# Performance work log

Hardware: AMD Instinct MI355X
Metric: run time of the kernel (lower is better)

Reference implementation:

```python
import jax, jax.numpy as jnp
import numpy as np

B, S, D, H, F, V = 64, 64, 512, 8, 2048, 8192
L = 6
ENC_C = 2048  # InceptionV3 feature channels
NEG_INF = jnp.float32(-jnp.inf)


def _layernorm(x, g, b, eps=1e-3):
    mu = jnp.mean(x, axis=-1, keepdims=True)
    var = jnp.var(x, axis=-1, keepdims=True)
    return (x - mu) * jax.lax.rsqrt(var + eps) * g + b


def _mha(q_in, kv_in, Wq, Wk, Wv, Wo, causal=False):
    Bq, Sq, Dm = q_in.shape
    Sk = kv_in.shape[1]
    dh = Dm // H
    q = (q_in @ Wq).reshape(Bq, Sq, H, dh)
    k = (kv_in @ Wk).reshape(Bq, Sk, H, dh)
    v = (kv_in @ Wv).reshape(Bq, Sk, H, dh)
    scores = jnp.einsum('bqhd,bkhd->bhqk', q, k) / jnp.sqrt(jnp.float32(dh))
    if causal:
        mask = jnp.tril(jnp.ones((Sq, Sk), dtype=bool))
        scores = jnp.where(mask, scores, jnp.float32(-1e9))
    a = jax.nn.softmax(scores, axis=-1)
    o = jnp.einsum('bhqk,bkhd->bqhd', a, v).reshape(Bq, Sq, Dm)
    return o @ Wo


def replacement_mask(targets):
    # out[b,i,v] = -inf iff some j<=i has targets[b,j]==v and v!=0
    valid = (targets != 0)[..., None].astype(jnp.float32)  # (B,S,1)
    oh = jax.nn.one_hot(targets, V, dtype=jnp.float32) * valid  # (B,S,V)
    seen = jnp.cumsum(oh, axis=1) > 0
    return jnp.where(seen, NEG_INF, jnp.float32(0.0))


def setup_inputs() -> dict:
    key = jax.random.key(0)
    ks = jax.random.split(key, 32)
    n = lambda i, shp, sc=0.02: jax.random.normal(ks[i], shp, jnp.float32) * sc
    inp = {
        'enc_feat': jax.random.normal(ks[0], (B, 8, 8, ENC_C), jnp.float32),
        'targets': jax.random.randint(ks[1], (B, S), 0, V, jnp.int32),
        'conv_w': n(2, (ENC_C, D)), 'conv_b': jnp.zeros((D,), jnp.float32),
        'tok_emb': n(3, (V, D)), 'pos_emb': n(4, (S, D)),
        'Wq_s': n(5, (L, D, D)), 'Wk_s': n(6, (L, D, D)),
        'Wv_s': n(7, (L, D, D)), 'Wo_s': n(8, (L, D, D)),
        'Wq_c': n(9, (L, D, D)), 'Wk_c': n(10, (L, D, D)),
        'Wv_c': n(11, (L, D, D)), 'Wo_c': n(12, (L, D, D)),
        'W1': n(13, (L, D, F)), 'fb1': jnp.zeros((L, F), jnp.float32),
        'W2': n(14, (L, F, D)), 'fb2': jnp.zeros((L, D), jnp.float32),
        'g1': jnp.ones((L, D), jnp.float32), 'be1': jnp.zeros((L, D), jnp.float32),
        'g2': jnp.ones((L, D), jnp.float32), 'be2': jnp.zeros((L, D), jnp.float32),
        'g3': jnp.ones((L, D), jnp.float32), 'be3': jnp.zeros((L, D), jnp.float32),
        'Wout': n(15, (D, V)), 'bout': jnp.zeros((V,), jnp.float32),
    }
    return inp


def reference(enc_feat, conv_w, conv_b, tok_emb, pos_emb,
              Wq_s, Wk_s, Wv_s, Wo_s, Wq_c, Wk_c, Wv_c, Wo_c,
              W1, fb1, W2, fb2, g1, be1, g2, be2, g3, be3,
              Wout, bout, targets):
    # 1x1 conv == per-pixel matmul, then flatten spatial -> (B, 64, D)
    enc = enc_feat.reshape(B, -1, ENC_C) @ conv_w + conv_b
    # decoder: token + positional embedding
    x = tok_emb[targets] + pos_emb[None, :, :]
    for l in range(L):
        a1 = _mha(x, x, Wq_s[l], Wk_s[l], Wv_s[l], Wo_s[l], causal=True)
        x = _layernorm(x + a1, g1[l], be1[l])
        a2 = _mha(x, enc, Wq_c[l], Wk_c[l], Wv_c[l], Wo_c[l])
        x = _layernorm(x + a2, g2[l], be2[l])
        ff = jax.nn.relu(x @ W1[l] + fb1[l]) @ W2[l] + fb2[l]
        x = _layernorm(x + ff, g3[l], be3[l])
    logits = x @ Wout + bout
    return logits + replacement_mask(targets)
```

## Files before the change

### kernel.cpp

```cpp
#include <hip/hip_runtime.h>
#include <cstdint>
#include <cstddef>

#define SS   64
#define BB   64
#define DM   512
#define NH   8
#define DH   64
#define FF   2048
#define VV   8192
#define LL   6
#define ENCC 2048
#define MR   4096

#define MASK_SENTINEL -3.0e38f

typedef unsigned short u16;
typedef __attribute__((ext_vector_type(8))) short bf16x8;
typedef __attribute__((ext_vector_type(4))) float f32x4;

__device__ __forceinline__ u16 f2b(float f) {
    union { float f; uint32_t u; } c; c.f = f;
    uint32_t u = c.u;
    return (u16)((u + 0x7fffu + ((u >> 16) & 1u)) >> 16);
}
__device__ __forceinline__ float blo(uint32_t p) {
    union { uint32_t u; float f; } c; c.u = p << 16; return c.f;
}
__device__ __forceinline__ float bhi(uint32_t p) {
    union { uint32_t u; float f; } c; c.u = p & 0xffff0000u; return c.f;
}

#define GLL(g, l) __builtin_amdgcn_global_load_lds( \
    (const __attribute__((address_space(1))) void*)(g), \
    (__attribute__((address_space(3))) void*)(l), 16, 0, 0)

#define WAITV2 asm volatile("s_waitcnt vmcnt(2)" ::: "memory")
#define WAITV3 asm volatile("s_waitcnt vmcnt(3)" ::: "memory")
#define WAITV4 asm volatile("s_waitcnt vmcnt(4)" ::: "memory")
#define WAITV0 asm volatile("s_waitcnt vmcnt(0)" ::: "memory")
#define WAITL0 asm volatile("s_waitcnt lgkmcnt(0)" ::: "memory")

template<int BMT, int BNT>
__global__ __launch_bounds__(256) void gemm_bf16(
    const u16* __restrict__ A, const u16* __restrict__ BT,
    const float* __restrict__ bias, u16* __restrict__ Cb,
    int K, int ldc, int relu)
{
    constexpr int WNW = (BNT == 128) ? 2 : 1;
    constexpr int WMW = 4 / WNW;
    constexpr int WM = BMT / WMW;
    constexpr int AI = WM / 16;
    constexpr int AG = BMT / 64;
    constexpr int BG = BNT / 64;
    constexpr int G  = AG + BG;
    constexpr int TILE = (BMT + BNT) * 32;
    __shared__ __align__(16) u16 smem[3 * TILE];
    const int tid = threadIdx.x;
    const int wave = tid >> 6, lane = tid & 63;

    const int m0 = blockIdx.y * BMT, n0 = blockIdx.x * BNT;
    const int srow = wave * 16 + (lane >> 2);
    const int scol = (lane & 3) * 8;
    const u16* Ap  = A  + (size_t)(m0 + srow) * K + scol;
    const u16* Bp  = BT + (size_t)(n0 + srow) * K + scol;
    const u16* Ap2 = Ap + (size_t)64 * K;
    const u16* Bp2 = Bp + (size_t)64 * K;
    const int aW = wave * 16 * 32;
    const int bW = BMT * 32 + wave * 16 * 32;

    const int wm = (BNT == 128) ? (wave >> 1) : wave;
    const int wn = (BNT == 128) ? (wave & 1) : 0;
    const int q = lane >> 4, mr = lane & 15;
    const int aRd = (wm * WM + mr) * 32 + q * 8;
    const int bRd = BMT * 32 + (wn * 64 + mr) * 32 + q * 8;

    f32x4 acc[AI][4];
    const f32x4 z = {0.f, 0.f, 0.f, 0.f};
#pragma unroll
    for (int i = 0; i < AI; i++)
#pragma unroll
        for (int j = 0; j < 4; j++) acc[i][j] = z;

#define STAGE(buf) do { \
        GLL(Ap, (buf) + aW); \
        if constexpr (AG == 2) GLL(Ap2, (buf) + aW + 64 * 32); \
        GLL(Bp, (buf) + bW); \
        if constexpr (BG == 2) GLL(Bp2, (buf) + bW + 64 * 32); \
        Ap += 32; Bp += 32; \
        if constexpr (AG == 2) Ap2 += 32; \
        if constexpr (BG == 2) Bp2 += 32; \
    } while (0)

    u16* rd = smem;
    u16* md = smem + TILE;
    u16* pf = smem + 2 * TILE;
    STAGE(rd);
    STAGE(md);
    const int NS = K >> 5;

    for (int k = 0; k < NS - 1; k++) {
        if constexpr (G == 2) WAITV2;
        else if constexpr (G == 3) WAITV3;
        else WAITV4;
        __builtin_amdgcn_s_barrier();
        bf16x8 af[AI], bfr[4];
#pragma unroll
        for (int i = 0; i < AI; i++) af[i]  = *(const bf16x8*)(rd + aRd + i * 16 * 32);
#pragma unroll
        for (int j = 0; j < 4; j++) bfr[j] = *(const bf16x8*)(rd + bRd + j * 16 * 32);
        WAITL0;
        __builtin_amdgcn_sched_barrier(0);
        if (k + 2 < NS) STAGE(pf);
#pragma unroll
        for (int i = 0; i < AI; i++)
#pragma unroll
            for (int j = 0; j < 4; j++)
                acc[i][j] = __builtin_amdgcn_mfma_f32_16x16x32_bf16(af[i], bfr[j], acc[i][j], 0, 0, 0);
        u16* t = rd; rd = md; md = pf; pf = t;
    }
    WAITV0;
    __builtin_amdgcn_s_barrier();
    {
        bf16x8 af[AI], bfr[4];
#pragma unroll
        for (int i = 0; i < AI; i++) af[i]  = *(const bf16x8*)(rd + aRd + i * 16 * 32);
#pragma unroll
        for (int j = 0; j < 4; j++) bfr[j] = *(const bf16x8*)(rd + bRd + j * 16 * 32);
#pragma unroll
        for (int i = 0; i < AI; i++)
#pragma unroll
            for (int j = 0; j < 4; j++)
                acc[i][j] = __builtin_amdgcn_mfma_f32_16x16x32_bf16(af[i], bfr[j], acc[i][j], 0, 0, 0);
    }
    __syncthreads();
#undef STAGE

    float* ep = (float*)smem + wave * 1024;
    const int lq = lane >> 4, lmr = lane & 15;
    const int colb = n0 + wn * 64 + lmr * 4;
    float4 b4 = make_float4(0.f, 0.f, 0.f, 0.f);
    if (bias) b4 = *(const float4*)(bias + colb);
#pragma unroll
    for (int i = 0; i < AI; i++) {
#pragma unroll
        for (int j = 0; j < 4; j++)
#pragma unroll
            for (int r = 0; r < 4; r++)
                ep[(q * 4 + r) * 64 + j * 16 + mr] = acc[i][j][r];
        __syncthreads();
#pragma unroll
        for (int p = 0; p < 4; p++) {
            const int lr = p * 4 + lq;
            float4 v = *(const float4*)(ep + lr * 64 + lmr * 4);
            v.x += b4.x; v.y += b4.y; v.z += b4.z; v.w += b4.w;
            if (relu) {
                v.x = fmaxf(v.x, 0.f); v.y = fmaxf(v.y, 0.f);
                v.z = fmaxf(v.z, 0.f); v.w = fmaxf(v.w, 0.f);
            }
            uint2 pk;
            pk.x = (uint32_t)f2b(v.x) | ((uint32_t)f2b(v.y) << 16);
            pk.y = (uint32_t)f2b(v.z) | ((uint32_t)f2b(v.w) << 16);
            const int row = m0 + wm * WM + i * 16 + lr;
            *(uint2*)(Cb + (size_t)row * ldc + colb) = pk;
        }
        __syncthreads();
    }
}

__global__ __launch_bounds__(256) void gemm_logits_mfma(
    const u16* __restrict__ A, const u16* __restrict__ BT,
    const float* __restrict__ bias, const int* __restrict__ fo,
    float* __restrict__ C, int K)
{
    constexpr int TILE = 256 * 32;
    __shared__ __align__(16) u16 smem[3 * TILE];
    const int tid = threadIdx.x;
    const int wave = tid >> 6, lane = tid & 63;
    const int m0 = blockIdx.y * 128, n0 = blockIdx.x * 128;

    const int srow = wave * 16 + (lane >> 2);
    const int scol = (lane & 3) * 8;
    const u16* Ap  = A  + (size_t)(m0 + srow) * K + scol;
    const u16* Bp  = BT + (size_t)(n0 + srow) * K + scol;
    const u16* Ap2 = Ap + (size_t)64 * K;
    const u16* Bp2 = Bp + (size_t)64 * K;
    const int aW = wave * 16 * 32;
    const int bW = 128 * 32 + wave * 16 * 32;

    const int wm = wave >> 1, wn = wave & 1;
    const int q = lane >> 4, mr = lane & 15;
    const int aRd = (wm * 64 + mr) * 32 + q * 8;
    const int bRd = 128 * 32 + (wn * 64 + mr) * 32 + q * 8;

    f32x4 acc[4][4];
    const f32x4 z = {0.f, 0.f, 0.f, 0.f};
#pragma unroll
    for (int i = 0; i < 4; i++)
#pragma unroll
        for (int j = 0; j < 4; j++) acc[i][j] = z;

#define STAGE4(buf) do { \
        GLL(Ap,  (buf) + aW); \
        GLL(Ap2, (buf) + aW + 64 * 32); \
        GLL(Bp,  (buf) + bW); \
        GLL(Bp2, (buf) + bW + 64 * 32); \
        Ap += 32; Ap2 += 32; Bp += 32; Bp2 += 32; \
    } while (0)

    u16* rd = smem;
    u16* md = smem + TILE;
    u16* pf = smem + 2 * TILE;
    STAGE4(rd);
    STAGE4(md);
    const int NS = K >> 5;

    for (int k = 0; k < NS - 1; k++) {
        WAITV4;
        __builtin_amdgcn_s_barrier();
        bf16x8 af[4], bfr[4];
#pragma unroll
        for (int i = 0; i < 4; i++) af[i]  = *(const bf16x8*)(rd + aRd + i * 16 * 32);
#pragma unroll
        for (int j = 0; j < 4; j++) bfr[j] = *(const bf16x8*)(rd + bRd + j * 16 * 32);
        WAITL0;
        __builtin_amdgcn_sched_barrier(0);
        if (k + 2 < NS) STAGE4(pf);
#pragma unroll
        for (int i = 0; i < 4; i++)
#pragma unroll
            for (int j = 0; j < 4; j++)
                acc[i][j] = __builtin_amdgcn_mfma_f32_16x16x32_bf16(af[i], bfr[j], acc[i][j], 0, 0, 0);
        u16* t = rd; rd = md; md = pf; pf = t;
    }
    WAITV0;
    __builtin_amdgcn_s_barrier();
    {
        bf16x8 af[4], bfr[4];
#pragma unroll
        for (int i = 0; i < 4; i++) af[i]  = *(const bf16x8*)(rd + aRd + i * 16 * 32);
#pragma unroll
        for (int j = 0; j < 4; j++) bfr[j] = *(const bf16x8*)(rd + bRd + j * 16 * 32);
#pragma unroll
        for (int i = 0; i < 4; i++)
#pragma unroll
            for (int j = 0; j < 4; j++)
                acc[i][j] = __builtin_amdgcn_mfma_f32_16x16x32_bf16(af[i], bfr[j], acc[i][j], 0, 0, 0);
    }
    __syncthreads();
#undef STAGE4

    float* ep = (float*)smem + wave * 1024;
    const int lq = lane >> 4, lmr = lane & 15;
    const int colb = n0 + wn * 64 + lmr * 4;
    const float4 b4 = *(const float4*)(bias + colb);
#pragma unroll
    for (int i = 0; i < 4; i++) {
#pragma unroll
        for (int j = 0; j < 4; j++)
#pragma unroll
            for (int r = 0; r < 4; r++)
                ep[(q * 4 + r) * 64 + j * 16 + mr] = acc[i][j][r];
        __syncthreads();
#pragma unroll
        for (int p = 0; p < 4; p++) {
            const int lr = p * 4 + lq;
            const int row = m0 + wm * 64 + i * 16 + lr;
            const int b = row >> 6, pos = row & 63;
            float4 v = *(const float4*)(ep + lr * 64 + lmr * 4);
            const int4 f4 = *(const int4*)(fo + (size_t)b * VV + colb);
            v.x = (f4.x <= pos) ? MASK_SENTINEL : v.x + b4.x;
            v.y = (f4.y <= pos) ? MASK_SENTINEL : v.y + b4.y;
            v.z = (f4.z <= pos) ? MASK_SENTINEL : v.z + b4.z;
            v.w = (f4.w <= pos) ? MASK_SENTINEL : v.w + b4.w;
            *(float4*)(C + (size_t)row * VV + colb) = v;
        }
        __syncthreads();
    }
}

struct TPB {
    const float* s[8];
    u16* d[8];
    long dz[8];
};

__global__ __launch_bounds__(256) void transpose8_kernel(TPB t)
{
    __shared__ float tl[32][33];
    const int zz = blockIdx.z;
    const int m = zz / 6, l = zz - m * 6;
    const float* in = t.s[m] + (size_t)l * 262144;
    u16* out = t.d[m] + (size_t)l * t.dz[m];
    const int r0 = blockIdx.y * 32, c0 = blockIdx.x * 32;
    const int tx = threadIdx.x & 31, ty = threadIdx.x >> 5;
#pragma unroll
    for (int i = 0; i < 4; i++)
        tl[ty + 8 * i][tx] = in[(size_t)(r0 + ty + 8 * i) * 512 + c0 + tx];
    __syncthreads();
#pragma unroll
    for (int i = 0; i < 4; i++)
        out[(size_t)(c0 + ty + 8 * i) * 512 + r0 + tx] = f2b(tl[tx][ty + 8 * i]);
}

__global__ __launch_bounds__(256) void transpose_bf16_kernel(
    const float* __restrict__ in, u16* __restrict__ out,
    int R, int C, size_t in_z, size_t out_z)
{
    __shared__ float tl[32][33];
    in  += (size_t)blockIdx.z * in_z;
    out += (size_t)blockIdx.z * out_z;
    const int r0 = blockIdx.y * 32, c0 = blockIdx.x * 32;
    const int tx = threadIdx.x & 31, ty = threadIdx.x >> 5;
#pragma unroll
    for (int i = 0; i < 4; i++)
        tl[ty + 8 * i][tx] = in[(size_t)(r0 + ty + 8 * i) * C + c0 + tx];
    __syncthreads();
#pragma unroll
    for (int i = 0; i < 4; i++)
        out[(size_t)(c0 + ty + 8 * i) * R + r0 + tx] = f2b(tl[tx][ty + 8 * i]);
}

__global__ __launch_bounds__(256) void convert_bf16_kernel(
    const float* __restrict__ in, u16* __restrict__ out)
{
    const int idx = blockIdx.x * 256 + threadIdx.x;
    float4 v = *reinterpret_cast<const float4*>(in + (size_t)idx * 4);
    uint2 p;
    p.x = (uint32_t)f2b(v.x) | ((uint32_t)f2b(v.y) << 16);
    p.y = (uint32_t)f2b(v.z) | ((uint32_t)f2b(v.w) << 16);
    *reinterpret_cast<uint2*>(out + (size_t)idx * 4) = p;
}

__global__ __launch_bounds__(256) void attn_kernel(
    const u16* __restrict__ qg, int qld,
    const u16* __restrict__ kg, const u16* __restrict__ vg, int kvld,
    u16* __restrict__ og, int causal)
{
    __shared__ float qs[SS][68];
    __shared__ float ks[SS][68];
    __shared__ float vs[SS][68];
    __shared__ float red[SS][8];
    float (*ps)[68] = qs;

    const int tid = threadIdx.x;
    const int bh = blockIdx.x;
    const int b = bh >> 3, h = bh & 7;
    const size_t qbase = (size_t)b * SS * qld + (size_t)h * DH;
    const size_t kbase = (size_t)b * SS * kvld + (size_t)h * DH;
    const size_t obase = (size_t)b * SS * DM + (size_t)h * DH;

#pragma unroll
    for (int it = 0; it < 4; it++) {
        int idx = tid + 256 * it;
        int s = idx >> 4;
        int d4 = (idx & 15) << 2;
        uint2 a = *(const uint2*)(qg + qbase + (size_t)s * qld + d4);
        qs[s][d4 + 0] = blo(a.x); qs[s][d4 + 1] = bhi(a.x);
        qs[s][d4 + 2] = blo(a.y); qs[s][d4 + 3] = bhi(a.y);
        uint2 c = *(const uint2*)(kg + kbase + (size_t)s * kvld + d4);
        ks[s][d4 + 0] = blo(c.x); ks[s][d4 + 1] = bhi(c.x);
        ks[s][d4 + 2] = blo(c.y); ks[s][d4 + 3] = bhi(c.y);
        uint2 e = *(const uint2*)(vg + kbase + (size_t)s * kvld + d4);
        vs[s][d4 + 0] = blo(e.x); vs[s][d4 + 1] = bhi(e.x);
        vs[s][d4 + 2] = blo(e.y); vs[s][d4 + 3] = bhi(e.y);
    }
    __syncthreads();

    const int r = tid >> 2, c = tid & 3;

    float sc[16];
#pragma unroll
    for (int jj = 0; jj < 16; jj++) sc[jj] = 0.f;
    for (int d4 = 0; d4 < 64; d4 += 4) {
        float4 qv = *reinterpret_cast<const float4*>(&qs[r][d4]);
#pragma unroll
        for (int jj = 0; jj < 16; jj++) {
            int j = jj * 4 + c;
            float4 kv = *reinterpret_cast<const float4*>(&ks[j][d4]);
            sc[jj] += qv.x * kv.x + qv.y * kv.y + qv.z * kv.z + qv.w * kv.w;
        }
    }
    float mx = -1e30f;
#pragma unroll
    for (int jj = 0; jj < 16; jj++) {
        int j = jj * 4 + c;
        float s_ = sc[jj] * 0.125f;
        if (causal && j > r) s_ = -1e9f;
        sc[jj] = s_;
        mx = fmaxf(mx, s_);
    }
    red[r][c] = mx;
    __syncthreads();
    float m = fmaxf(fmaxf(red[r][0], red[r][1]), fmaxf(red[r][2], red[r][3]));
    float sum = 0.f;
#pragma unroll
    for (int jj = 0; jj < 16; jj++) {
        float p = expf(sc[jj] - m);
        sc[jj] = p;
        sum += p;
    }
    red[r][4 + c] = sum;
    __syncthreads();
    float tot = red[r][4] + red[r][5] + red[r][6] + red[r][7];
    float inv = 1.f / tot;
#pragma unroll
    for (int jj = 0; jj < 16; jj++) ps[r][jj * 4 + c] = sc[jj] * inv;
    __syncthreads();

    float acc[16];
#pragma unroll
    for (int i = 0; i < 16; i++) acc[i] = 0.f;
    for (int j = 0; j < 64; j++) {
        float pj = ps[r][j];
#pragma unroll
        for (int dd = 0; dd < 4; dd++) {
            float4 vv = *reinterpret_cast<const float4*>(&vs[j][c * 16 + dd * 4]);
            acc[dd * 4 + 0] += pj * vv.x;
            acc[dd * 4 + 1] += pj * vv.y;
            acc[dd * 4 + 2] += pj * vv.z;
            acc[dd * 4 + 3] += pj * vv.w;
        }
    }
#pragma unroll
    for (int dd = 0; dd < 4; dd++) {
        uint2 p;
        p.x = (uint32_t)f2b(acc[dd * 4 + 0]) | ((uint32_t)f2b(acc[dd * 4 + 1]) << 16);
        p.y = (uint32_t)f2b(acc[dd * 4 + 2]) | ((uint32_t)f2b(acc[dd * 4 + 3]) << 16);
        *reinterpret_cast<uint2*>(&og[obase + (size_t)r * DM + c * 16 + dd * 4]) = p;
    }
}

__global__ __launch_bounds__(256) void add_ln_kernel(
    const float* __restrict__ x, const u16* __restrict__ a,
    const float* __restrict__ g, const float* __restrict__ be,
    float* __restrict__ y, u16* __restrict__ yb)
{
    const int wave = threadIdx.x >> 6, lane = threadIdx.x & 63;
    const int row = blockIdx.x * 4 + wave;
    const float* xr = x + (size_t)row * DM;
    const u16* ar = a + (size_t)row * DM;
    float* yr = y + (size_t)row * DM;
    u16* ybr = yb + (size_t)row * DM;

    float vbuf[8];
    float sum = 0.f, sq = 0.f;
#pragma unroll
    for (int i = 0; i < 2; i++) {
        int d = lane * 8 + i * 4;
        float4 xv = *reinterpret_cast<const float4*>(&xr[d]);
        uint2 av = *(const uint2*)(ar + d);
        float a0 = blo(av.x), a1 = bhi(av.x), a2 = blo(av.y), a3 = bhi(av.y);
        float v0 = xv.x + a0, v1 = xv.y + a1, v2 = xv.z + a2, v3 = xv.w + a3;
        vbuf[i * 4 + 0] = v0; vbuf[i * 4 + 1] = v1;
        vbuf[i * 4 + 2] = v2; vbuf[i * 4 + 3] = v3;
        sum += v0 + v1 + v2 + v3;
        sq += v0 * v0 + v1 * v1 + v2 * v2 + v3 * v3;
    }
#pragma unroll
    for (int off = 32; off; off >>= 1) {
        sum += __shfl_xor(sum, off, 64);
        sq  += __shfl_xor(sq, off, 64);
    }
    float mean = sum * (1.f / 512.f);
    float var = sq * (1.f / 512.f) - mean * mean;
    float rs = rsqrtf(var + 1e-3f);
#pragma unroll
    for (int i = 0; i < 2; i++) {
        int d = lane * 8 + i * 4;
        float4 gv = *reinterpret_cast<const float4*>(&g[d]);
        float4 bv = *reinterpret_cast<const float4*>(&be[d]);
        float4 ov;
        ov.x = (vbuf[i * 4 + 0] - mean) * rs * gv.x + bv.x;
        ov.y = (vbuf[i * 4 + 1] - mean) * rs * gv.y + bv.y;
        ov.z = (vbuf[i * 4 + 2] - mean) * rs * gv.z + bv.z;
        ov.w = (vbuf[i * 4 + 3] - mean) * rs * gv.w + bv.w;
        *reinterpret_cast<float4*>(&yr[d]) = ov;
        uint2 p;
        p.x = (uint32_t)f2b(ov.x) | ((uint32_t)f2b(ov.y) << 16);
        p.y = (uint32_t)f2b(ov.z) | ((uint32_t)f2b(ov.w) << 16);
        *reinterpret_cast<uint2*>(&ybr[d]) = p;
    }
}

__global__ __launch_bounds__(256) void embed_kernel(
    const int* __restrict__ targets, const float* __restrict__ tok,
    const float* __restrict__ pos, float* __restrict__ x, u16* __restrict__ xb)
{
    int idx = blockIdx.x * 256 + threadIdx.x;
    int row = idx >> 7;
    int d4 = (idx & 127) << 2;
    int s = row & 63;
    int t = targets[row];
    float4 tv = *reinterpret_cast<const float4*>(&tok[(size_t)t * DM + d4]);
    float4 pv = *reinterpret_cast<const float4*>(&pos[(size_t)s * DM + d4]);
    float4 ov = make_float4(tv.x + pv.x, tv.y + pv.y, tv.z + pv.z, tv.w + pv.w);
    *reinterpret_cast<float4*>(&x[(size_t)row * DM + d4]) = ov;
    uint2 p;
    p.x = (uint32_t)f2b(ov.x) | ((uint32_t)f2b(ov.y) << 16);
    p.y = (uint32_t)f2b(ov.z) | ((uint32_t)f2b(ov.w) << 16);
    *reinterpret_cast<uint2*>(&xb[(size_t)row * DM + d4]) = p;
}

__global__ __launch_bounds__(256) void init_fo_kernel(int* __restrict__ fo)
{
    fo[blockIdx.x * 256 + threadIdx.x] = SS;
}

__global__ __launch_bounds__(256) void scatter_fo_kernel(
    const int* __restrict__ targets, int* __restrict__ fo)
{
    int i = blockIdx.x * 256 + threadIdx.x;
    int t = targets[i];
    if (t != 0) atomicMin(&fo[(size_t)(i >> 6) * VV + t], i & 63);
}

extern "C" void kernel_launch(void* const* d_in, const int* in_sizes, int n_in,
                              void* d_out, int out_size, void* d_ws, size_t ws_size,
                              hipStream_t stream)
{
    const float* enc_feat = (const float*)d_in[0];
    const int*   targets  = (const int*)d_in[1];
    const float* conv_w   = (const float*)d_in[2];
    const float* conv_b   = (const float*)d_in[3];
    const float* tok_emb  = (const float*)d_in[4];
    const float* pos_emb  = (const float*)d_in[5];
    const float* Wq_s     = (const float*)d_in[6];
    const float* Wk_s     = (const float*)d_in[7];
    const float* Wv_s     = (const float*)d_in[8];
    const float* Wo_s     = (const float*)d_in[9];
    const float* Wq_c     = (const float*)d_in[10];
    const float* Wk_c     = (const float*)d_in[11];
    const float* Wv_c     = (const float*)d_in[12];
    const float* Wo_c     = (const float*)d_in[13];
    const float* W1       = (const float*)d_in[14];
    const float* fb1      = (const float*)d_in[15];
    const float* W2       = (const float*)d_in[16];
    const float* fb2      = (const float*)d_in[17];
    const float* g1       = (const float*)d_in[18];
    const float* be1      = (const float*)d_in[19];
    const float* g2       = (const float*)d_in[20];
    const float* be2      = (const float*)d_in[21];
    const float* g3       = (const float*)d_in[22];
    const float* be3      = (const float*)d_in[23];
    const float* Wout     = (const float*)d_in[24];
    const float* bout     = (const float*)d_in[25];
    float* out = (float*)d_out;

    u16* base = (u16*)d_ws;
    float* x   = (float*)d_ws;
    u16* xb    = base + 4194304;
    u16* projb = base + 6291456;
    u16* qcb   = base + 8388608;
    u16* attnb = base + 10485760;
    u16* encb  = base + 12582912;
    u16* big   = base + 14680064;
    int* fo    = (int*)(base + 23068672);
    u16* qkvT  = base + 24117248;
    u16* woTs  = base + 28835840;
    u16* wqTc  = base + 30408704;
    u16* kvTc  = base + 31981568;
    u16* woTc  = base + 35127296;
    u16* w1T   = base + 36700160;
    u16* w2T   = base + 42991616;
    u16* cvT   = base + 49283072;
    u16* woutT = base + 50331648;
    u16* kvAll = base + 54525952;

    const dim3 blk(256);

    init_fo_kernel<<<dim3(BB * VV / 256), blk, 0, stream>>>(fo);
    scatter_fo_kernel<<<dim3(MR / 256), blk, 0, stream>>>(targets, fo);
    embed_kernel<<<dim3(MR * DM / 4 / 256), blk, 0, stream>>>(targets, tok_emb, pos_emb, x, xb);
    convert_bf16_kernel<<<dim3(MR * ENCC / 4 / 256), blk, 0, stream>>>(enc_feat, big);

    TPB tp;
    tp.s[0] = Wq_s; tp.d[0] = qkvT;          tp.dz[0] = 786432;
    tp.s[1] = Wk_s; tp.d[1] = qkvT + 262144; tp.dz[1] = 786432;
    tp.s[2] = Wv_s; tp.d[2] = qkvT + 524288; tp.dz[2] = 786432;
    tp.s[3] = Wo_s; tp.d[3] = woTs;          tp.dz[3] = 262144;
    tp.s[4] = Wq_c; tp.d[4] = wqTc;          tp.dz[4] = 262144;
    tp.s[5] = Wk_c; tp.d[5] = kvTc;          tp.dz[5] = 524288;
    tp.s[6] = Wv_c; tp.d[6] = kvTc + 262144; tp.dz[6] = 524288;
    tp.s[7] = Wo_c; tp.d[7] = woTc;          tp.dz[7] = 262144;
    transpose8_kernel<<<dim3(16, 16, 48), blk, 0, stream>>>(tp);
    transpose_bf16_kernel<<<dim3(64, 16, 6), blk, 0, stream>>>(W1, w1T, 512, 2048, 1048576, 1048576);
    transpose_bf16_kernel<<<dim3(16, 64, 6), blk, 0, stream>>>(W2, w2T, 2048, 512, 1048576, 1048576);
    transpose_bf16_kernel<<<dim3(16, 64, 1), blk, 0, stream>>>(conv_w, cvT, 2048, 512, 0, 0);
    transpose_bf16_kernel<<<dim3(256, 16, 1), blk, 0, stream>>>(Wout, woutT, 512, 8192, 0, 0);

    gemm_bf16<64, 64><<<dim3(8, 64), blk, 0, stream>>>(big, cvT, conv_b, encb, ENCC, DM, 0);

    gemm_bf16<64, 128><<<dim3(48, 64), blk, 0, stream>>>(encb, kvTc, nullptr, kvAll, DM, 6144, 0);

    for (int l = 0; l < LL; l++) {
        gemm_bf16<64, 128><<<dim3(12, 64), blk, 0, stream>>>(xb, qkvT + (size_t)l * 786432, nullptr,
                                                             big, DM, 1536, 0);
        attn_kernel<<<dim3(BB * NH), blk, 0, stream>>>(big, 1536, big + 512, big + 1024, 1536, attnb, 1);
        gemm_bf16<64, 64><<<dim3(8, 64), blk, 0, stream>>>(attnb, woTs + (size_t)l * 262144, nullptr,
                                                           projb, DM, DM, 0);
        add_ln_kernel<<<dim3(MR / 4), blk, 0, stream>>>(x, projb, g1 + l * DM, be1 + l * DM, x, xb);
        gemm_bf16<64, 64><<<dim3(8, 64), blk, 0, stream>>>(xb, wqTc + (size_t)l * 262144, nullptr,
                                                           qcb, DM, DM, 0);
        attn_kernel<<<dim3(BB * NH), blk, 0, stream>>>(qcb, 512,
                                                       kvAll + (size_t)l * 1024,
                                                       kvAll + (size_t)l * 1024 + 512, 6144, attnb, 0);
        gemm_bf16<64, 64><<<dim3(8, 64), blk, 0, stream>>>(attnb, woTc + (size_t)l * 262144, nullptr,
                                                           projb, DM, DM, 0);
        add_ln_kernel<<<dim3(MR / 4), blk, 0, stream>>>(x, projb, g2 + l * DM, be2 + l * DM, x, xb);
        gemm_bf16<64, 128><<<dim3(16, 64), blk, 0, stream>>>(xb, w1T + (size_t)l * 1048576,
                                                             fb1 + (size_t)l * FF, big, DM, FF, 1);
        gemm_bf16<64, 64><<<dim3(8, 64), blk, 0, stream>>>(big, w2T + (size_t)l * 1048576,
                                                           fb2 + (size_t)l * DM, projb, FF, DM, 0);
        add_ln_kernel<<<dim3(MR / 4), blk, 0, stream>>>(x, projb, g3 + l * DM, be3 + l * DM, x, xb);
    }

    gemm_logits_mfma<<<dim3(64, 32), blk, 0, stream>>>(xb, woutT, bout, fo, out, DM);
}
```

Before: 1.240 ms.

## Double GEMM K-step to 64 and XOR-swizzle LDS tiles to avoid bank conflicts

```diff
diff --git a/kernel.cpp b/kernel.cpp
--- a/kernel.cpp
+++ b/kernel.cpp
@@ -35,10 +35,8 @@
     (const __attribute__((address_space(1))) void*)(g), \
     (__attribute__((address_space(3))) void*)(l), 16, 0, 0)
 
-#define WAITV2 asm volatile("s_waitcnt vmcnt(2)" ::: "memory")
-#define WAITV3 asm volatile("s_waitcnt vmcnt(3)" ::: "memory")
+#define WAITV0 asm volatile("s_waitcnt vmcnt(0)" ::: "memory")
 #define WAITV4 asm volatile("s_waitcnt vmcnt(4)" ::: "memory")
-#define WAITV0 asm volatile("s_waitcnt vmcnt(0)" ::: "memory")
 #define WAITL0 asm volatile("s_waitcnt lgkmcnt(0)" ::: "memory")
 
 template<int BMT, int BNT>
@@ -49,31 +47,31 @@
 {
     constexpr int WNW = (BNT == 128) ? 2 : 1;
     constexpr int WMW = 4 / WNW;
-    constexpr int WM = BMT / WMW;
-    constexpr int AI = WM / 16;
-    constexpr int AG = BMT / 64;
-    constexpr int BG = BNT / 64;
-    constexpr int G  = AG + BG;
-    constexpr int TILE = (BMT + BNT) * 32;
+    constexpr int WM  = BMT / WMW;
+    constexpr int AI  = WM / 16;
+    constexpr int AG  = BMT / 32;
+    constexpr int BG  = BNT / 32;
+    constexpr int G   = AG + BG;
+    constexpr int TILE = (BMT + BNT) * 64;
     __shared__ __align__(16) u16 smem[3 * TILE];
     const int tid = threadIdx.x;
     const int wave = tid >> 6, lane = tid & 63;
 
     const int m0 = blockIdx.y * BMT, n0 = blockIdx.x * BNT;
-    const int srow = wave * 16 + (lane >> 2);
-    const int scol = (lane & 3) * 8;
-    const u16* Ap  = A  + (size_t)(m0 + srow) * K + scol;
-    const u16* Bp  = BT + (size_t)(n0 + srow) * K + scol;
-    const u16* Ap2 = Ap + (size_t)64 * K;
-    const u16* Bp2 = Bp + (size_t)64 * K;
-    const int aW = wave * 16 * 32;
-    const int bW = BMT * 32 + wave * 16 * 32;
+
+    const int r8 = lane >> 3;
+    const int sc = ((lane & 7) ^ r8) * 8;
+    const u16* Ap = A  + (size_t)(m0 + wave * (AG * 8) + r8) * K + sc;
+    const u16* Bp = BT + (size_t)(n0 + wave * (BG * 8) + r8) * K + sc;
+    const int aW = wave * (AG * 8) * 64;
+    const int bW = BMT * 64 + wave * (BG * 8) * 64;
 
     const int wm = (BNT == 128) ? (wave >> 1) : wave;
     const int wn = (BNT == 128) ? (wave & 1) : 0;
     const int q = lane >> 4, mr = lane & 15;
-    const int aRd = (wm * WM + mr) * 32 + q * 8;
-    const int bRd = BMT * 32 + (wn * 64 + mr) * 32 + q * 8;
+    const int wmR = wm * WM;
+    const int sw0 = ((q)     ^ (mr & 7)) * 8;
+    const int sw1 = ((4 + q) ^ (mr & 7)) * 8;
 
     f32x4 acc[AI][4];
     const f32x4 z = {0.f, 0.f, 0.f, 0.f};
@@ -82,59 +80,78 @@
 #pragma unroll
         for (int j = 0; j < 4; j++) acc[i][j] = z;
 
-#define STAGE(buf) do { \
-        GLL(Ap, (buf) + aW); \
-        if constexpr (AG == 2) GLL(Ap2, (buf) + aW + 64 * 32); \
-        GLL(Bp, (buf) + bW); \
-        if constexpr (BG == 2) GLL(Bp2, (buf) + bW + 64 * 32); \
-        Ap += 32; Bp += 32; \
-        if constexpr (AG == 2) Ap2 += 32; \
-        if constexpr (BG == 2) Bp2 += 32; \
-    } while (0)
+    auto STAGE = [&](u16* buf) {
+#pragma unroll
+        for (int i = 0; i < AG; i++)
+            GLL(Ap + (size_t)(i * 8) * K, buf + aW + i * 8 * 64);
+#pragma unroll
+        for (int i = 0; i < BG; i++)
+            GLL(Bp + (size_t)(i * 8) * K, buf + bW + i * 8 * 64);
+        Ap += 64; Bp += 64;
+    };
 
     u16* rd = smem;
     u16* md = smem + TILE;
     u16* pf = smem + 2 * TILE;
     STAGE(rd);
     STAGE(md);
-    const int NS = K >> 5;
+    const int NS = K >> 6;
 
     for (int k = 0; k < NS - 1; k++) {
-        if constexpr (G == 2) WAITV2;
-        else if constexpr (G == 3) WAITV3;
-        else WAITV4;
+        if constexpr (G == 4) asm volatile("s_waitcnt vmcnt(4)" ::: "memory");
+        else if constexpr (G == 6) asm volatile("s_waitcnt vmcnt(6)" ::: "memory");
+        else asm volatile("s_waitcnt vmcnt(8)" ::: "memory");
         __builtin_amdgcn_s_barrier();
-        bf16x8 af[AI], bfr[4];
-#pragma unroll
-        for (int i = 0; i < AI; i++) af[i]  = *(const bf16x8*)(rd + aRd + i * 16 * 32);
-#pragma unroll
-        for (int j = 0; j < 4; j++) bfr[j] = *(const bf16x8*)(rd + bRd + j * 16 * 32);
+        bf16x8 a0[AI], a1[AI], b0[4], b1[4];
+#pragma unroll
+        for (int i = 0; i < AI; i++) {
+            const u16* p = rd + (wmR + i * 16 + mr) * 64;
+            a0[i] = *(const bf16x8*)(p + sw0);
+            a1[i] = *(const bf16x8*)(p + sw1);
+        }
+#pragma unroll
+        for (int j = 0; j < 4; j++) {
+            const u16* p = rd + BMT * 64 + (wn * 64 + j * 16 + mr) * 64;
+            b0[j] = *(const bf16x8*)(p + sw0);
+            b1[j] = *(const bf16x8*)(p + sw1);
+        }
         WAITL0;
         __builtin_amdgcn_sched_barrier(0);
         if (k + 2 < NS) STAGE(pf);
 #pragma unroll
         for (int i = 0; i < AI; i++)
 #pragma unroll
-            for (int j = 0; j < 4; j++)
-                acc[i][j] = __builtin_amdgcn_mfma_f32_16x16x32_bf16(af[i], bfr[j], acc[i][j], 0, 0, 0);
+            for (int j = 0; j < 4; j++) {
+                acc[i][j] = __builtin_amdgcn_mfma_f32_16x16x32_bf16(a0[i], b0[j], acc[i][j], 0, 0, 0);
+                acc[i][j] = __builtin_amdgcn_mfma_f32_16x16x32_bf16(a1[i], b1[j], acc[i][j], 0, 0, 0);
+            }
         u16* t = rd; rd = md; md = pf; pf = t;
     }
     WAITV0;
     __builtin_amdgcn_s_barrier();
     {
-        bf16x8 af[AI], bfr[4];
-#pragma unroll
-        for (int i = 0; i < AI; i++) af[i]  = *(const bf16x8*)(rd + aRd + i * 16 * 32);
-#pragma unroll
-        for (int j = 0; j < 4; j++) bfr[j] = *(const bf16x8*)(rd + bRd + j * 16 * 32);
+        bf16x8 a0[AI], a1[AI], b0[4], b1[4];
+#pragma unroll
+        for (int i = 0; i < AI; i++) {
+            const u16* p = rd + (wmR + i * 16 + mr) * 64;
+            a0[i] = *(const bf16x8*)(p + sw0);
+            a1[i] = *(const bf16x8*)(p + sw1);
+        }
+#pragma unroll
+        for (int j = 0; j < 4; j++) {
+            const u16* p = rd + BMT * 64 + (wn * 64 + j * 16 + mr) * 64;
+            b0[j] = *(const bf16x8*)(p + sw0);
+            b1[j] = *(const bf16x8*)(p + sw1);
+        }
 #pragma unroll
         for (int i = 0; i < AI; i++)
 #pragma unroll
-            for (int j = 0; j < 4; j++)
-                acc[i][j] = __builtin_amdgcn_mfma_f32_16x16x32_bf16(af[i], bfr[j], acc[i][j], 0, 0, 0);
-    }
-    __syncthreads();
-#undef STAGE
+            for (int j = 0; j < 4; j++) {
+                acc[i][j] = __builtin_amdgcn_mfma_f32_16x16x32_bf16(a0[i], b0[j], acc[i][j], 0, 0, 0);
+                acc[i][j] = __builtin_amdgcn_mfma_f32_16x16x32_bf16(a1[i], b1[j], acc[i][j], 0, 0, 0);
+            }
+    }
+    __syncthreads();
 
     float* ep = (float*)smem + wave * 1024;
     const int lq = lane >> 4, lmr = lane & 15;
@@ -180,7 +197,7 @@
     const int m0 = blockIdx.y * 128, n0 = blockIdx.x * 128;
 
     const int srow = wave * 16 + (lane >> 2);
-    const int scol = (lane & 3) * 8;
+    const int scol = ((lane & 3) ^ ((lane >> 3) & 3)) * 8;
     const u16* Ap  = A  + (size_t)(m0 + srow) * K + scol;
     const u16* Bp  = BT + (size_t)(n0 + srow) * K + scol;
     const u16* Ap2 = Ap + (size_t)64 * K;
@@ -190,8 +207,9 @@
 
     const int wm = wave >> 1, wn = wave & 1;
     const int q = lane >> 4, mr = lane & 15;
-    const int aRd = (wm * 64 + mr) * 32 + q * 8;
-    const int bRd = 128 * 32 + (wn * 64 + mr) * 32 + q * 8;
+    const int swz = (q ^ ((mr >> 1) & 3)) * 8;
+    const int aRd = (wm * 64 + mr) * 32 + swz;
+    const int bRd = 128 * 32 + (wn * 64 + mr) * 32 + swz;
 
     f32x4 acc[4][4];
     const f32x4 z = {0.f, 0.f, 0.f, 0.f};
```

Measured after the change: 1.229 ms. Within noise of the previous version (-0.9%).
